# Kernel optimization log

Measured on AMD Instinct MI355X. Metric: run time of the kernel, lower is better.

The kernel has to match this reference:

```python
import jax, jax.numpy as jnp
import numpy as np

ALPHA = 0.2  # leakyrelu slope


def setup_inputs() -> dict:
    key = jax.random.key(0)
    ks = jax.random.split(key, 10)
    B, L, F, H, D = 16, 1024, 128, 4, 64
    HD = H * D  # 256
    s = lambda fan: 1.0 / np.sqrt(fan)
    return {
        "x":  jax.random.normal(ks[0], (B, L, F), jnp.float32),
        "W":  jax.random.normal(ks[1], (H, F, D), jnp.float32) * s(F),
        "a1": jax.random.normal(ks[2], (H, D), jnp.float32) * s(2 * D),
        "a2": jax.random.normal(ks[3], (H, D), jnp.float32) * s(2 * D),
        "Wq": jax.random.normal(ks[4], (HD, HD), jnp.float32) * s(HD),
        "bq": jnp.zeros((HD,), jnp.float32),
        "Wk": jax.random.normal(ks[5], (HD, HD), jnp.float32) * s(HD),
        "bk": jnp.zeros((HD,), jnp.float32),
        "Wv": jax.random.normal(ks[6], (HD, HD), jnp.float32) * s(HD),
        "bv": jnp.zeros((HD,), jnp.float32),
        "Wfc": jax.random.normal(ks[7], (HD, D), jnp.float32) * s(HD),
        "bfc": jnp.zeros((D,), jnp.float32),
    }


def reference(x, W, a1, a2, Wq, bq, Wk, bk, Wv, bv, Wfc, bfc):
    # ---- multi-head GAT (dense, all-pairs over seq_len) ----
    # Wh: [H, B, L, D]
    Wh = jnp.einsum('blf,hfd->hbld', x, W)
    # e_ij = leakyrelu(a1.Wh_i + a2.Wh_j)  (split of a over the concat)
    si = jnp.einsum('hbld,hd->hbl', Wh, a1)  # source term
    sj = jnp.einsum('hbld,hd->hbl', Wh, a2)  # target term
    e = jax.nn.leaky_relu(si[..., :, None] + sj[..., None, :], negative_slope=ALPHA)
    gat_att = jax.nn.softmax(e, axis=-1)               # [H,B,L,L]
    # dropout is identity in eval mode (training=False)
    h = jnp.einsum('hblm,hbmd->hbld', gat_att, Wh)     # [H,B,L,D]
    # concat heads -> [B, L, H*D]
    Hh, B, L, D = h.shape
    gat_out = jnp.transpose(h, (1, 2, 0, 3)).reshape(B, L, Hh * D)

    # ---- temporal attention over the concatenated features ----
    Q = gat_out @ Wq + bq
    K = gat_out @ Wk + bk
    V = gat_out @ Wv + bv
    scale = 1.0 / np.sqrt(Hh * D)
    scores = jnp.einsum('bld,bmd->blm', Q, K) * scale
    t_att = jax.nn.softmax(scores, axis=-1)            # [B,L,L]
    temporal_out = jnp.einsum('blm,bmd->bld', t_att, V)

    # ---- output projection (dropout identity in eval) ----
    out = temporal_out @ Wfc + bfc                     # [B,L,D]
    return (out, gat_att, t_att, temporal_out)
```

## Files before the change

### kernel.cpp

```cpp
#include <hip/hip_runtime.h>


constexpr int Bc = 16, Lc = 1024, Fc = 128, Hc = 4, Dc = 64, HDc = 256;
constexpr int Nrows = Bc * Lc;
#define ALPHA_SLOPE 0.2f

typedef __attribute__((ext_vector_type(8))) short bf16x8;
typedef __attribute__((ext_vector_type(4))) float f32x4;

enum { A_F32 = 0, A_HL = 1 };
enum { E_BIAS = 1, E_WHT = 2, E_STATS = 3, E_QKV = 4 };

__device__ __forceinline__ float lrelu(float x) { return x > 0.f ? x : ALPHA_SLOPE * x; }

__device__ __forceinline__ void gll16(const void* g, void* l) {
    __builtin_amdgcn_global_load_lds(
        (const __attribute__((address_space(1))) void*)g,
        (__attribute__((address_space(3))) void*)l, 16, 0, 0);
}

__device__ __forceinline__ void split2(float a, float b, unsigned& h, unsigned& l) {
    const unsigned ua = __float_as_uint(a), ub = __float_as_uint(b);
    h = __byte_perm(ua, ub, 0x7632);
    const float la = a - __uint_as_float(ua & 0xffff0000u);
    const float lb = b - __uint_as_float(ub & 0xffff0000u);
    l = __byte_perm(__float_as_uint(la), __float_as_uint(lb), 0x7632);
}
__device__ __forceinline__ void split1(float v, unsigned short& h, unsigned short& l) {
    const unsigned u = __float_as_uint(v);
    h = (unsigned short)(u >> 16);
    const float lf = v - __uint_as_float(u & 0xffff0000u);
    l = (unsigned short)(__float_as_uint(lf) >> 16);
}

template <int BM, int BN, int AMODE, int EPI>
__global__ __launch_bounds__(256, 2) void mm_k(
    const float* __restrict__ Af,
    const unsigned short* __restrict__ Agh, const unsigned short* __restrict__ Agl,
    const unsigned short* __restrict__ Bgh, const unsigned short* __restrict__ Bgl,
    const float* __restrict__ bias,
    float* __restrict__ Cf,
    unsigned short* __restrict__ Ch, unsigned short* __restrict__ Cl,
    unsigned short* __restrict__ Ch2, unsigned short* __restrict__ Cl2,
    unsigned short* __restrict__ Ch3, unsigned short* __restrict__ Cl3,
    int K, int lda, int ldb, int ldc,
    long long zA, long long zB, long long zC, float alpha,
    const float* __restrict__ a1, const float* __restrict__ a2,
    float* __restrict__ si, float* __restrict__ sj, float* __restrict__ pstats)
{
    constexpr int ABUF = BM * 32, BBUF = BN * 32;
    __shared__ __align__(16) unsigned short SM[4 * ABUF + 4 * BBUF];
    unsigned short* const Ah_s = SM;
    unsigned short* const Al_s = SM + 2 * ABUF;
    unsigned short* const Bh_s = SM + 4 * ABUF;
    unsigned short* const Bl_s = SM + 4 * ABUF + 2 * BBUF;

    constexpr bool SWAPXY = (EPI == E_QKV);

    const int nbx = gridDim.x, nby = gridDim.y;
    int lin = blockIdx.x + nbx * (blockIdx.y + nby * blockIdx.z);
    const int ntot = nbx * nby * gridDim.z;
    lin = (lin & 7) * (ntot >> 3) + (lin >> 3);
    const int bx = lin % nbx;
    const int rem = lin / nbx;
    const int by = rem % nby;
    const int z  = rem / nby;

    if (AMODE == A_F32) { Af += (size_t)z * zA; }
    else { Agh += (size_t)z * zA; Agl += (size_t)z * zA; }
    Bgh += (size_t)z * zB; Bgl += (size_t)z * zB;
    if (Cf) Cf += (size_t)z * zC;

    constexpr int WC = (BN == 64) ? 1 : 2, WR = 4 / WC;
    constexpr int WM = BM / WR, WN = BN / WC, MF = WM / 16, NF = WN / 16;
    const int row0 = (SWAPXY ? by : bx) * BM;
    const int col0 = (SWAPXY ? bx : by) * BN;
    const int t = threadIdx.x, lane = t & 63, wid = t >> 6;
    const int fr = lane & 15, g = lane >> 4, fk = g * 8;
    const int wrow = (wid / WC) * WM, wcol = (wid % WC) * WN;
    const int rsub = lane >> 2, cbyt = (lane & 3) * 16;

    f32x4 acc[MF][NF] = {};

    auto stageB = [&](int k0, int pp) {
        #pragma unroll
        for (int q = 0; q < BN / 64; ++q) {
            const int r = wid * (BN / 4) + q * 16;
            const size_t gb = ((size_t)(col0 + r + rsub) * ldb + k0) * 2 + cbyt;
            gll16((const char*)Bgh + gb, (char*)(Bh_s + pp * BBUF) + (size_t)r * 64);
            gll16((const char*)Bgl + gb, (char*)(Bl_s + pp * BBUF) + (size_t)r * 64);
        }
    };
    auto stageA = [&](int k0, int pp) {
        if (AMODE == A_HL) {
            #pragma unroll
            for (int q = 0; q < BM / 64; ++q) {
                const int r = wid * (BM / 4) + q * 16;
                const size_t gb = ((size_t)(row0 + r + rsub) * lda + k0) * 2 + cbyt;
                gll16((const char*)Agh + gb, (char*)(Ah_s + pp * ABUF) + (size_t)r * 64);
                gll16((const char*)Agl + gb, (char*)(Al_s + pp * ABUF) + (size_t)r * 64);
            }
        } else {
            const int r = t >> 1, h2 = t & 1;
            const float* srcA = Af + (size_t)(row0 + r) * lda + k0 + h2 * 16;
            const float4 v0 = ((const float4*)srcA)[0];
            const float4 v1 = ((const float4*)srcA)[1];
            const float4 v2 = ((const float4*)srcA)[2];
            const float4 v3 = ((const float4*)srcA)[3];
            unsigned hu[8], lu[8];
            split2(v0.x, v0.y, hu[0], lu[0]); split2(v0.z, v0.w, hu[1], lu[1]);
            split2(v1.x, v1.y, hu[2], lu[2]); split2(v1.z, v1.w, hu[3], lu[3]);
            split2(v2.x, v2.y, hu[4], lu[4]); split2(v2.z, v2.w, hu[5], lu[5]);
            split2(v3.x, v3.y, hu[6], lu[6]); split2(v3.z, v3.w, hu[7], lu[7]);
            uint4* dh = (uint4*)(Ah_s + pp * ABUF + r * 32 + h2 * 16);
            dh[0] = make_uint4(hu[0], hu[1], hu[2], hu[3]);
            dh[1] = make_uint4(hu[4], hu[5], hu[6], hu[7]);
            uint4* dl = (uint4*)(Al_s + pp * ABUF + r * 32 + h2 * 16);
            dl[0] = make_uint4(lu[0], lu[1], lu[2], lu[3]);
            dl[1] = make_uint4(lu[4], lu[5], lu[6], lu[7]);
        }
    };

    stageB(0, 0);
    stageA(0, 0);
    __syncthreads();

    const int NT = K / 32;
    int p = 0;
    for (int kt = 0; kt < NT; ++kt) {
        if (kt + 1 < NT) { stageB((kt + 1) * 32, p ^ 1); stageA((kt + 1) * 32, p ^ 1); }
        bf16x8 ah[MF], al[MF];
        #pragma unroll
        for (int mf = 0; mf < MF; ++mf) {
            const int off = p * ABUF + (wrow + mf * 16 + fr) * 32 + fk;
            ah[mf] = *(const bf16x8*)(Ah_s + off);
            al[mf] = *(const bf16x8*)(Al_s + off);
        }
        #pragma unroll
        for (int nf = 0; nf < NF; ++nf) {
            const int off = p * BBUF + (wcol + nf * 16 + fr) * 32 + fk;
            const bf16x8 bh = *(const bf16x8*)(Bh_s + off);
            const bf16x8 bl = *(const bf16x8*)(Bl_s + off);
            #pragma unroll
            for (int mf = 0; mf < MF; ++mf) {
                acc[mf][nf] = __builtin_amdgcn_mfma_f32_16x16x32_bf16(ah[mf], bh, acc[mf][nf], 0, 0, 0);
                acc[mf][nf] = __builtin_amdgcn_mfma_f32_16x16x32_bf16(al[mf], bh, acc[mf][nf], 0, 0, 0);
                acc[mf][nf] = __builtin_amdgcn_mfma_f32_16x16x32_bf16(ah[mf], bl, acc[mf][nf], 0, 0, 0);
            }
        }
        __syncthreads();
        p ^= 1;
    }

    float* ts = (float*)SM;

    if (EPI == E_BIAS || EPI == E_STATS) {
        float bv_[NF];
        if (EPI == E_BIAS) {
            #pragma unroll
            for (int nf = 0; nf < NF; ++nf) bv_[nf] = bias[col0 + wcol + nf * 16 + fr];
        }
        #pragma unroll
        for (int mf = 0; mf < MF; ++mf) {
            #pragma unroll
            for (int i = 0; i < 4; ++i) {
                const size_t row = (size_t)row0 + wrow + mf * 16 + g * 4 + i;
                const size_t co = row * ldc + col0 + wcol + fr;
                #pragma unroll
                for (int nf = 0; nf < NF; ++nf) {
                    float v = acc[mf][nf][i];
                    if (EPI == E_STATS) v *= alpha;
                    if (EPI == E_BIAS)  v += bv_[nf];
                    acc[mf][nf][i] = v;
                    Cf[co + nf * 16] = v;
                }
            }
        }
        if (EPI == E_STATS) {
            const int ty = by * WC + (wid % WC);
            #pragma unroll
            for (int mf = 0; mf < MF; ++mf) {
                #pragma unroll
                for (int i = 0; i < 4; ++i) {
                    float m = acc[mf][0][i], s;
                    #pragma unroll
                    for (int nf = 1; nf < NF; ++nf) m = fmaxf(m, acc[mf][nf][i]);
                    s = 0.f;
                    #pragma unroll
                    for (int nf = 0; nf < NF; ++nf) s += __expf(acc[mf][nf][i] - m);
                    #pragma unroll
                    for (int ofs = 1; ofs < 16; ofs <<= 1) {
                        const float om = __shfl_xor(m, ofs, 64);
                        const float os = __shfl_xor(s, ofs, 64);
                        const float nm = fmaxf(m, om);
                        s = s * __expf(m - nm) + os * __expf(om - nm);
                        m = nm;
                    }
                    if (fr == 0) {
                        const size_t row = (size_t)row0 + wrow + mf * 16 + g * 4 + i;
                        float* pp = pstats + (((size_t)z * 16 + ty) * Lc + row) * 2;
                        pp[0] = m; pp[1] = s;
                    }
                }
            }
        }
    }

    if (EPI == E_QKV) {
        float bv_[NF];
        #pragma unroll
        for (int nf = 0; nf < NF; ++nf) bv_[nf] = bias[col0 + wcol + nf * 16 + fr];
        #pragma unroll
        for (int mf = 0; mf < MF; ++mf)
            #pragma unroll
            for (int i = 0; i < 4; ++i)
                #pragma unroll
                for (int nf = 0; nf < NF; ++nf) acc[mf][nf][i] += bv_[nf];

        if (col0 < 512) {
            unsigned short* dH = (col0 < 256) ? Ch : Ch2;
            unsigned short* dL = (col0 < 256) ? Cl : Cl2;
            const int cl0 = col0 & 255;
            #pragma unroll
            for (int mf = 0; mf < MF; ++mf) {
                #pragma unroll
                for (int i = 0; i < 4; ++i) {
                    const size_t row = (size_t)row0 + wrow + mf * 16 + g * 4 + i;
                    const size_t co = row * ldc + cl0 + wcol + fr;
                    #pragma unroll
                    for (int nf = 0; nf < NF; ++nf) {
                        unsigned short hh16, ll16; split1(acc[mf][nf][i], hh16, ll16);
                        dH[co + nf * 16] = hh16; dL[co + nf * 16] = ll16;
                    }
                }
            }
        } else {
            const int bq_ = row0 >> 10, lg0 = row0 & 1023;
            #pragma unroll
            for (int hf = 0; hf < 2; ++hf) {
                if ((wid & 1) == hf) {
                    #pragma unroll
                    for (int mf = 0; mf < MF; ++mf)
                        #pragma unroll
                        for (int i = 0; i < 4; ++i) {
                            const int rr = wrow + mf * 16 + g * 4 + i;
                            #pragma unroll
                            for (int nf = 0; nf < NF; ++nf)
                                ts[rr * 65 + nf * 16 + fr] = acc[mf][nf][i];
                        }
                }
                __syncthreads();
                const int l = t & 127, db = (t >> 7) * 32;
                #pragma unroll
                for (int dd = 0; dd < 32; ++dd) {
                    const int dl = db + dd;
                    unsigned short hh16, ll16; split1(ts[l * 65 + dl], hh16, ll16);
                    const size_t o = ((size_t)bq_ * 256 + (col0 - 512) + hf * 64 + dl) * 1024 + lg0 + l;
                    Ch3[o] = hh16; Cl3[o] = ll16;
                }
                __syncthreads();
            }
        }
    }

    if (EPI == E_WHT) {
        float a1v[NF], a2v[NF];
        #pragma unroll
        for (int nf = 0; nf < NF; ++nf) {
            a1v[nf] = a1[(size_t)z * Dc + nf * 16 + fr];
            a2v[nf] = a2[(size_t)z * Dc + nf * 16 + fr];
        }
        #pragma unroll
        for (int mf = 0; mf < MF; ++mf) {
// ... 20 lines not shown
        #pragma unroll
        for (int mf = 0; mf < MF; ++mf)
            #pragma unroll
            for (int i = 0; i < 4; ++i) {
                const int rr = wrow + mf * 16 + g * 4 + i;
                #pragma unroll
                for (int nf = 0; nf < NF; ++nf)
                    ts[rr * 65 + nf * 16 + fr] = acc[mf][nf][i];
            }
        __syncthreads();
        const int bq_ = row0 >> 10, lg0 = row0 & 1023;
        const int l = t & 127, db = (t >> 7) * 32;
        #pragma unroll
        for (int dd = 0; dd < 32; ++dd) {
            const int d = db + dd;
            unsigned short hh16, ll16; split1(ts[l * 65 + d], hh16, ll16);
            const size_t o = (((size_t)(z * 16 + bq_)) * 64 + d) * 1024 + lg0 + l;
            Ch[o] = hh16; Cl[o] = ll16;
        }
    }
}

__global__ __launch_bounds__(256, 3) void gat_k(
    const float* __restrict__ si, const float* __restrict__ sj,
    const unsigned short* __restrict__ WhTh, const unsigned short* __restrict__ WhTl,
    float* __restrict__ att, unsigned short* __restrict__ gouth,
    unsigned short* __restrict__ goutl)
{
    constexpr int BBUF = 64 * 32;
    __shared__ __align__(16) unsigned short SMg[4 * BBUF];
    __shared__ __align__(16) float sjs[Lc];
    __shared__ float redm[4];
    unsigned short* const Bh_s = SMg;
    unsigned short* const Bl_s = SMg + 2 * BBUF;

    int lin = blockIdx.x + 8 * blockIdx.z;
    lin = (lin & 7) * 64 + (lin >> 3);
    const int bx = lin & 7, z = lin >> 3;

    const int row0 = bx * 128;
    const int t = threadIdx.x, lane = t & 63, wid = t >> 6;
    const int fr = lane & 15, g = lane >> 4, fk = g * 8;
    const int wrow = wid * 32;
    const int hh = z >> 4, bb = z & 15;
    const int rsub = lane >> 2, cbyt = (lane & 3) * 16;

    const unsigned short* WhTh_z = WhTh + (size_t)z * 64 * 1024;
    const unsigned short* WhTl_z = WhTl + (size_t)z * 64 * 1024;
    const float* sjz = sj + (size_t)z * 1024;
    float* attz = att + ((size_t)z * 1024 + row0) * 1024;

    auto stageB = [&](int j0, int pp) {
        const int r = wid * 16;
        const size_t gb = ((size_t)(r + rsub) * 1024 + j0) * 2 + cbyt;
        gll16((const char*)WhTh_z + gb, (char*)(Bh_s + pp * BBUF) + (size_t)r * 64);
        gll16((const char*)WhTl_z + gb, (char*)(Bl_s + pp * BBUF) + (size_t)r * 64);
    };

    stageB(0, 0);
    ((float4*)sjs)[t] = ((const float4*)sjz)[t];
    __syncthreads();

    {
        const float4 v = ((const float4*)sjs)[t];
        float m4 = fmaxf(fmaxf(v.x, v.y), fmaxf(v.z, v.w));
        #pragma unroll
        for (int ofs = 32; ofs >= 1; ofs >>= 1) m4 = fmaxf(m4, __shfl_xor(m4, ofs, 64));
        if (lane == 0) redm[wid] = m4;
    }
    __syncthreads();
    const float smax = fmaxf(fmaxf(redm[0], redm[1]), fmaxf(redm[2], redm[3]));
// ... 11 lines not shown
        for (int c = 0; c < 64; ++c) {
            const float4 w = sp[c];
            s += __expf(lrelu(sv + w.x) - mr[mf]) + __expf(lrelu(sv + w.y) - mr[mf])
               + __expf(lrelu(sv + w.z) - mr[mf]) + __expf(lrelu(sv + w.w) - mr[mf]);
        }
        s += __shfl_xor(s, 16, 64);
        s += __shfl_xor(s, 32, 64);
        inv[mf] = 1.0f / s;
    }

    f32x4 acc[2][4] = {};
    int p = 0;
    for (int kt = 0; kt < 32; ++kt) {
        const int j0 = kt * 32;
        if (kt < 31) stageB(j0 + 32, p ^ 1);
        bf16x8 ph[2], pl[2];
        #pragma unroll
        for (int mf = 0; mf < 2; ++mf) {
            const float4 s0 = ((const float4*)sjs)[(j0 >> 2) + g * 2];
            const float4 s1 = ((const float4*)sjs)[(j0 >> 2) + g * 2 + 1];
            float pr[8];
            pr[0] = __expf(lrelu(siv[mf] + s0.x) - mr[mf]) * inv[mf];
            pr[1] = __expf(lrelu(siv[mf] + s0.y) - mr[mf]) * inv[mf];
            pr[2] = __expf(lrelu(siv[mf] + s0.z) - mr[mf]) * inv[mf];
            pr[3] = __expf(lrelu(siv[mf] + s0.w) - mr[mf]) * inv[mf];
            pr[4] = __expf(lrelu(siv[mf] + s1.x) - mr[mf]) * inv[mf];
            pr[5] = __expf(lrelu(siv[mf] + s1.y) - mr[mf]) * inv[mf];
            pr[6] = __expf(lrelu(siv[mf] + s1.z) - mr[mf]) * inv[mf];
            pr[7] = __expf(lrelu(siv[mf] + s1.w) - mr[mf]) * inv[mf];
            float* ap = attz + (size_t)(wrow + mf * 16 + fr) * 1024 + j0 + fk;
            *(float4*)ap       = make_float4(pr[0], pr[1], pr[2], pr[3]);
            *(float4*)(ap + 4) = make_float4(pr[4], pr[5], pr[6], pr[7]);
            union { unsigned u[4]; bf16x8 v; } uh, ul;
            split2(pr[0], pr[1], uh.u[0], ul.u[0]);
            split2(pr[2], pr[3], uh.u[1], ul.u[1]);
            split2(pr[4], pr[5], uh.u[2], ul.u[2]);
            split2(pr[6], pr[7], uh.u[3], ul.u[3]);
            ph[mf] = uh.v; pl[mf] = ul.v;
        }
        #pragma unroll
        for (int nf = 0; nf < 4; ++nf) {
            const int off = p * BBUF + (nf * 16 + fr) * 32 + fk;
            const bf16x8 bh = *(const bf16x8*)(Bh_s + off);
            const bf16x8 bl = *(const bf16x8*)(Bl_s + off);
            #pragma unroll
            for (int mf = 0; mf < 2; ++mf) {
                acc[mf][nf] = __builtin_amdgcn_mfma_f32_16x16x32_bf16(ph[mf], bh, acc[mf][nf], 0, 0, 0);
                acc[mf][nf] = __builtin_amdgcn_mfma_f32_16x16x32_bf16(pl[mf], bh, acc[mf][nf], 0, 0, 0);
                acc[mf][nf] = __builtin_amdgcn_mfma_f32_16x16x32_bf16(ph[mf], bl, acc[mf][nf], 0, 0, 0);
            }
        }
        __syncthreads();
        p ^= 1;
    }
    #pragma unroll
    for (int mf = 0; mf < 2; ++mf) {
        #pragma unroll
        for (int i = 0; i < 4; ++i) {
            const int row_l = wrow + mf * 16 + g * 4 + i;
            const size_t base = ((size_t)bb * 1024 + row0 + row_l) * 256 + hh * 64 + fr;
            #pragma unroll
            for (int nf = 0; nf < 4; ++nf) {
                unsigned short hh16, ll16; split1(acc[mf][nf][i], hh16, ll16);
                gouth[base + nf * 16] = hh16;
                goutl[base + nf * 16] = ll16;
            }
        }
    }
}

__global__ __launch_bounds__(256, 2) void pv_k(
    float* __restrict__ scores, const float* __restrict__ pstats,
    const unsigned short* __restrict__ VTh, const unsigned short* __restrict__ VTl,
    const unsigned short* __restrict__ WfcTh, const unsigned short* __restrict__ WfcTl,
    const float* __restrict__ bfc,
    float* __restrict__ tout, float* __restrict__ outp)
{
    constexpr int ABUF = 32 * 32, BBUF = 256 * 32;
    __shared__ __align__(16) unsigned short SMp[4 * ABUF + 4 * BBUF];
    unsigned short* const Ah_s = SMp;
    unsigned short* const Al_s = SMp + 2 * ABUF;
    unsigned short* const Bh_s = SMp + 4 * ABUF;
    unsigned short* const Bl_s = SMp + 4 * ABUF + 2 * BBUF;

    int lin = blockIdx.x + 32 * blockIdx.z;
    lin = (lin & 7) * 64 + (lin >> 3);
    const int bx = lin & 31, z = lin >> 5;

    const int row0 = bx * 32;
    const int t = threadIdx.x, lane = t & 63, wid = t >> 6;
    const int fr = lane & 15, g = lane >> 4, fk = g * 8;
    const int rsub = lane >> 2, cbyt = (lane & 3) * 16;

    float* sc = scores + ((size_t)z * Lc + row0) * Lc;
    const unsigned short* VTh_z = VTh + (size_t)z * HDc * Lc;
    const unsigned short* VTl_z = VTl + (size_t)z * HDc * Lc;

    auto stageB = [&](int k0, int pp) {
        #pragma unroll
        for (int q = 0; q < 4; ++q) {
            const int r = q * 64 + wid * 16;
            const size_t gb = ((size_t)(r + rsub) * Lc + k0) * 2 + cbyt;
            gll16((const char*)VTh_z + gb, (char*)(Bh_s + pp * BBUF) + (size_t)r * 64);
            gll16((const char*)VTl_z + gb, (char*)(Bl_s + pp * BBUF) + (size_t)r * 64);
        }
    };

    stageB(0, 0);

    const int ar = t >> 3, cq = (t & 7) * 4;
    float m_ = -1e30f, s_ = 0.f;
    {
        const int q = t & 7;
        const float* pb = pstats + (((size_t)z * 16 + q * 2) * Lc + row0 + ar) * 2;
        #pragma unroll
        for (int j = 0; j < 2; ++j) {
            const float2 pp = *(const float2*)(pb + (size_t)j * Lc * 2);
            const float nm = fmaxf(m_, pp.x);
            s_ = s_ * __expf(m_ - nm) + pp.y * __expf(pp.x - nm);
// ... 6 lines not shown
            const float nm = fmaxf(m_, om);
            s_ = s_ * __expf(m_ - nm) + os * __expf(om - nm);
            m_ = nm;
        }
    }
    const float iv_ = 1.0f / s_;

    auto stageA = [&](int k0, int pp) {
        float* srcS = sc + (size_t)ar * Lc + k0 + cq;
        const float4 v0 = *(const float4*)srcS;
        float pr[4];
        pr[0] = __expf(v0.x - m_) * iv_; pr[1] = __expf(v0.y - m_) * iv_;
        pr[2] = __expf(v0.z - m_) * iv_; pr[3] = __expf(v0.w - m_) * iv_;
        *(float4*)srcS = make_float4(pr[0], pr[1], pr[2], pr[3]);
        unsigned hu[2], lu[2];
        split2(pr[0], pr[1], hu[0], lu[0]); split2(pr[2], pr[3], hu[1], lu[1]);
        *(uint2*)(Ah_s + pp * ABUF + ar * 32 + cq) = make_uint2(hu[0], hu[1]);
        *(uint2*)(Al_s + pp * ABUF + ar * 32 + cq) = make_uint2(lu[0], lu[1]);
    };

    f32x4 acc[2][4] = {};
    stageA(0, 0);
    __syncthreads();
    int p = 0;
    for (int kt = 0; kt < 32; ++kt) {
        if (kt < 31) { stageB((kt + 1) * 32, p ^ 1); stageA((kt + 1) * 32, p ^ 1); }
        bf16x8 ah[2], al[2];
        #pragma unroll
        for (int mf = 0; mf < 2; ++mf) {
            const int off = p * ABUF + (mf * 16 + fr) * 32 + fk;
            ah[mf] = *(const bf16x8*)(Ah_s + off);
            al[mf] = *(const bf16x8*)(Al_s + off);
        }
        #pragma unroll
        for (int nf = 0; nf < 4; ++nf) {
            const int off = p * BBUF + (wid * 64 + nf * 16 + fr) * 32 + fk;
            const bf16x8 bh = *(const bf16x8*)(Bh_s + off);
            const bf16x8 bl = *(const bf16x8*)(Bl_s + off);
            #pragma unroll
            for (int mf = 0; mf < 2; ++mf) {
                acc[mf][nf] = __builtin_amdgcn_mfma_f32_16x16x32_bf16(ah[mf], bh, acc[mf][nf], 0, 0, 0);
                acc[mf][nf] = __builtin_amdgcn_mfma_f32_16x16x32_bf16(al[mf], bh, acc[mf][nf], 0, 0, 0);
                acc[mf][nf] = __builtin_amdgcn_mfma_f32_16x16x32_bf16(ah[mf], bl, acc[mf][nf], 0, 0, 0);
            }
        }
        __syncthreads();
        p ^= 1;
    }

    constexpr int TS = 258;
    float* ts = (float*)SMp;
    #pragma unroll
    for (int mf = 0; mf < 2; ++mf) {
        #pragma unroll
        for (int i = 0; i < 4; ++i) {
            const size_t row = (size_t)row0 + mf * 16 + g * 4 + i;
            float* cp = tout + ((size_t)z * Lc + row) * HDc + wid * 64 + fr;
            #pragma unroll
            for (int nf = 0; nf < 4; ++nf) {
                cp[nf * 16] = acc[mf][nf][i];
                ts[(mf * 16 + g * 4 + i) * TS + wid * 64 + nf * 16 + fr] = acc[mf][nf][i];
            }
        }
    }
    __syncthreads();

    const int ocol = wid * 16 + fr;
    f32x4 acc2[2] = {};
    #pragma unroll
    for (int kt2 = 0; kt2 < 8; ++kt2) {
        const int kk = kt2 * 32 + fk;
        const bf16x8 bh = *(const bf16x8*)(WfcTh + ocol * 256 + kk);
        const bf16x8 bl = *(const bf16x8*)(WfcTl + ocol * 256 + kk);
        #pragma unroll
        for (int mf = 0; mf < 2; ++mf) {
            const float* ap = ts + (mf * 16 + fr) * TS + kk;
            union { unsigned u[4]; bf16x8 v; } ahh, all_;
            split2(ap[0], ap[1], ahh.u[0], all_.u[0]);
            split2(ap[2], ap[3], ahh.u[1], all_.u[1]);
            split2(ap[4], ap[5], ahh.u[2], all_.u[2]);
            split2(ap[6], ap[7], ahh.u[3], all_.u[3]);
            acc2[mf] = __builtin_amdgcn_mfma_f32_16x16x32_bf16(ahh.v, bh, acc2[mf], 0, 0, 0);
            acc2[mf] = __builtin_amdgcn_mfma_f32_16x16x32_bf16(all_.v, bh, acc2[mf], 0, 0, 0);
            acc2[mf] = __builtin_amdgcn_mfma_f32_16x16x32_bf16(ahh.v, bl, acc2[mf], 0, 0, 0);
        }
    }
    const float bo = bfc[ocol];
    #pragma unroll
    for (int mf = 0; mf < 2; ++mf)
        #pragma unroll
        for (int i = 0; i < 4; ++i)
            outp[((size_t)z * Lc + row0 + mf * 16 + g * 4 + i) * Dc + ocol] = acc2[mf][i] + bo;
}

__device__ __forceinline__ void tr32(const float* src, unsigned short* dh,
                                     unsigned short* dl, int R, int C,
                                     int r0, int c0, float (*tile)[33], int t)
{
    const int tc = t & 31, tr = t >> 5;
    #pragma unroll
    for (int rr = 0; rr < 32; rr += 8)
        tile[tr + rr][tc] = src[(size_t)(r0 + tr + rr) * C + c0 + tc];
    __syncthreads();
    #pragma unroll
    for (int rr = 0; rr < 32; rr += 8) {
        unsigned short h, l; split1(tile[tc][tr + rr], h, l);
        const size_t o = (size_t)(c0 + tr + rr) * R + r0 + tc;
        dh[o] = h; dl[o] = l;
    }
}

__global__ __launch_bounds__(256) void prep_k(
    const float* __restrict__ W, const float* __restrict__ Wq,
    const float* __restrict__ Wk, const float* __restrict__ Wv,
    const float* __restrict__ Wfc, const float* __restrict__ bq,
    const float* __restrict__ bk, const float* __restrict__ bv,
    unsigned short* __restrict__ WTh, unsigned short* __restrict__ WTl,
    unsigned short* __restrict__ Wch, unsigned short* __restrict__ Wcl,
    unsigned short* __restrict__ WfcTh, unsigned short* __restrict__ WfcTl,
    float* __restrict__ bcat)
{
    __shared__ float tile[32][33];
    const int bx = blockIdx.x, by = blockIdx.y, t = threadIdx.x;
    if (by == 0) {
        if (bx >= 32) return;
        const int h = bx >> 3, tl = bx & 7;
        tr32(W + (size_t)h * Fc * Dc, WTh + (size_t)h * Dc * Fc,
             WTl + (size_t)h * Dc * Fc, Fc, Dc, (tl >> 1) * 32, (tl & 1) * 32, tile, t);
    } else if (by <= 3) {
        const float* s = (by == 1) ? Wq : (by == 2) ? Wk : Wv;
        const size_t off = (size_t)(by - 1) * HDc * HDc;
        tr32(s, Wch + off, Wcl + off, HDc, HDc, (bx >> 3) * 32, (bx & 7) * 32, tile, t);
    } else {
        if (bx < 16) {
            tr32(Wfc, WfcTh, WfcTl, HDc, Dc, (bx >> 1) * 32, (bx & 1) * 32, tile, t);
        } else if (bx == 16) {
            bcat[t] = bq[t]; bcat[256 + t] = bk[t]; bcat[512 + t] = bv[t];
        }
    }
}

extern "C" void kernel_launch(void* const* d_in, const int* in_sizes, int n_in,
                              void* d_out, int out_size, void* d_ws, size_t ws_size,
                              hipStream_t stream)
{
    const float* x   = (const float*)d_in[0];
    const float* W   = (const float*)d_in[1];
    const float* a1  = (const float*)d_in[2];
    const float* a2  = (const float*)d_in[3];
    const float* Wq  = (const float*)d_in[4];
    const float* bq  = (const float*)d_in[5];
    const float* Wk  = (const float*)d_in[6];
    const float* bk  = (const float*)d_in[7];
    const float* Wv  = (const float*)d_in[8];
    const float* bv  = (const float*)d_in[9];
    const float* Wfc = (const float*)d_in[10];
    const float* bfc = (const float*)d_in[11];

    float* outp    = (float*)d_out;
    float* gat_att = outp + (size_t)Bc * Lc * Dc;
    float* t_att   = gat_att + (size_t)Hc * Bc * Lc * Lc;
    float* t_out   = t_att + (size_t)Bc * Lc * Lc;

    constexpr size_t MB = 1024 * 1024;
    char* wsb = (char*)d_ws;
    unsigned short* WhTh = (unsigned short*)wsb;
    unsigned short* WhTl = WhTh + (size_t)64 * 64 * 1024;
    unsigned short* VTh = WhTh; unsigned short* VTl = WhTl;
    unsigned short* gouth = (unsigned short*)(wsb + 16 * MB);
    unsigned short* goutl = gouth + (size_t)Nrows * HDc;
    unsigned short* Qh = (unsigned short*)(wsb + 32 * MB);
    unsigned short* Ql = Qh + (size_t)Nrows * HDc;
    unsigned short* Kh = (unsigned short*)(wsb + 48 * MB);
    unsigned short* Kl = Kh + (size_t)Nrows * HDc;
    float* si  = (float*)(wsb + 64 * MB);
    float* sj  = si + Hc * Nrows;
    float* pstats = sj + Hc * Nrows;
    unsigned short* WTh = (unsigned short*)(pstats + (size_t)Bc * 16 * Lc * 2);
    unsigned short* WTl = WTh + Hc * Dc * Fc;
    unsigned short* Wch = WTl + Hc * Dc * Fc;
    unsigned short* Wcl = Wch + 768 * HDc;
    unsigned short* WfcTh = Wcl + 768 * HDc;
    unsigned short* WfcTl = WfcTh + Dc * HDc;
    float* bcat = (float*)(WfcTl + Dc * HDc);

    const dim3 blk(256);

    prep_k<<<dim3(64, 5), blk, 0, stream>>>(W, Wq, Wk, Wv, Wfc, bq, bk, bv,
        WTh, WTl, Wch, Wcl, WfcTh, WfcTl, bcat);

    mm_k<128, 64, A_F32, E_WHT><<<dim3(Nrows / 128, 1, Hc), blk, 0, stream>>>(
        x, nullptr, nullptr, WTh, WTl, nullptr, nullptr,
        WhTh, WhTl, nullptr, nullptr, nullptr, nullptr,
        Fc, Fc, Fc, 0, 0LL, (long long)Dc * Fc, 0LL, 1.f, a1, a2, si, sj, nullptr);

    gat_k<<<dim3(Lc / 128, 1, 64), blk, 0, stream>>>(si, sj,
        WhTh, WhTl, gat_att, gouth, goutl);

    mm_k<128, 128, A_HL, E_QKV><<<dim3(6, Nrows / 128, 1), blk, 0, stream>>>(
        nullptr, gouth, goutl, Wch, Wcl, bcat, nullptr,
        Qh, Ql, Kh, Kl, VTh, VTl,
        HDc, HDc, HDc, HDc, 0LL, 0LL, 0LL, 1.f, nullptr, nullptr, nullptr, nullptr, nullptr);

    mm_k<128, 128, A_HL, E_STATS><<<dim3(8, 8, Bc), blk, 0, stream>>>(
        nullptr, Qh, Ql, Kh, Kl, nullptr, t_att,
        nullptr, nullptr, nullptr, nullptr, nullptr, nullptr,
        HDc, HDc, HDc, Lc, (long long)Lc * HDc, (long long)Lc * HDc,
        (long long)Lc * Lc, 0.0625f, nullptr, nullptr, nullptr, nullptr, pstats);

    pv_k<<<dim3(32, 1, Bc), blk, 0, stream>>>(t_att, pstats, VTh, VTl,
        WfcTh, WfcTl, bfc, t_out, outp);
}
```

Before: 235.2 us.

## Switch split-bf16 3-pass MFMA to fp16 hi/lo A with single fp16 B operand

Replaces the bf16 hi/lo emulation of fp32 GEMMs (three MFMAs per tile) with fp16: the A operand stays split into hi/lo fp16 while the B operand (weights, Wh, K, V) is stored as a single fp16. This removes one of three MFMAs per step, halves B-side LDS and global traffic, and shrinks the workspace for Wh, K and V. The cost is lower precision on the B side (fp16 mantissa, limited range), which could break tolerance if values overflow or need more bits.

```diff
diff --git a/kernel.cpp b/kernel.cpp
--- a/kernel.cpp
+++ b/kernel.cpp
@@ -5,11 +5,11 @@
 constexpr int Nrows = Bc * Lc;
 #define ALPHA_SLOPE 0.2f
 
-typedef __attribute__((ext_vector_type(8))) short bf16x8;
+typedef __attribute__((ext_vector_type(8))) _Float16 f16x8;
 typedef __attribute__((ext_vector_type(4))) float f32x4;
 
 enum { A_F32 = 0, A_HL = 1 };
-enum { E_BIAS = 1, E_WHT = 2, E_STATS = 3, E_QKV = 4 };
+enum { E_WHT = 2, E_STATS = 3, E_QKV = 4 };
 
 __device__ __forceinline__ float lrelu(float x) { return x > 0.f ? x : ALPHA_SLOPE * x; }
 
@@ -19,41 +19,43 @@
         (__attribute__((address_space(3))) void*)l, 16, 0, 0);
 }
 
-__device__ __forceinline__ void split2(float a, float b, unsigned& h, unsigned& l) {
-    const unsigned ua = __float_as_uint(a), ub = __float_as_uint(b);
-    h = __byte_perm(ua, ub, 0x7632);
-    const float la = a - __uint_as_float(ua & 0xffff0000u);
-    const float lb = b - __uint_as_float(ub & 0xffff0000u);
-    l = __byte_perm(__float_as_uint(la), __float_as_uint(lb), 0x7632);
-}
-__device__ __forceinline__ void split1(float v, unsigned short& h, unsigned short& l) {
-    const unsigned u = __float_as_uint(v);
-    h = (unsigned short)(u >> 16);
-    const float lf = v - __uint_as_float(u & 0xffff0000u);
-    l = (unsigned short)(__float_as_uint(lf) >> 16);
+__device__ __forceinline__ unsigned short cv1(float v) {
+    union { _Float16 f; unsigned short u; } c; c.f = (_Float16)v; return c.u;
+}
+__device__ __forceinline__ void sp2(float a, float b, unsigned& h, unsigned& l) {
+    const _Float16 ha = (_Float16)a, hb = (_Float16)b;
+    union { _Float16 f[2]; unsigned u; } H, L;
+    H.f[0] = ha; H.f[1] = hb;
+    L.f[0] = (_Float16)(a - (float)ha);
+    L.f[1] = (_Float16)(b - (float)hb);
+    h = H.u; l = L.u;
+}
+__device__ __forceinline__ void sp1(float v, unsigned short& h, unsigned short& l) {
+    const _Float16 hv = (_Float16)v;
+    union { _Float16 f; unsigned short u; } H, L;
+    H.f = hv; L.f = (_Float16)(v - (float)hv);
+    h = H.u; l = L.u;
 }
 
 template <int BM, int BN, int AMODE, int EPI>
 __global__ __launch_bounds__(256, 2) void mm_k(
     const float* __restrict__ Af,
     const unsigned short* __restrict__ Agh, const unsigned short* __restrict__ Agl,
-    const unsigned short* __restrict__ Bgh, const unsigned short* __restrict__ Bgl,
+    const unsigned short* __restrict__ Bg,
     const float* __restrict__ bias,
     float* __restrict__ Cf,
     unsigned short* __restrict__ Ch, unsigned short* __restrict__ Cl,
-    unsigned short* __restrict__ Ch2, unsigned short* __restrict__ Cl2,
-    unsigned short* __restrict__ Ch3, unsigned short* __restrict__ Cl3,
+    unsigned short* __restrict__ Ch2, unsigned short* __restrict__ Ch3,
     int K, int lda, int ldb, int ldc,
     long long zA, long long zB, long long zC, float alpha,
     const float* __restrict__ a1, const float* __restrict__ a2,
     float* __restrict__ si, float* __restrict__ sj, float* __restrict__ pstats)
 {
     constexpr int ABUF = BM * 32, BBUF = BN * 32;
-    __shared__ __align__(16) unsigned short SM[4 * ABUF + 4 * BBUF];
+    __shared__ __align__(16) unsigned short SM[4 * ABUF + 2 * BBUF];
     unsigned short* const Ah_s = SM;
     unsigned short* const Al_s = SM + 2 * ABUF;
-    unsigned short* const Bh_s = SM + 4 * ABUF;
-    unsigned short* const Bl_s = SM + 4 * ABUF + 2 * BBUF;
+    unsigned short* const Bf_s = SM + 4 * ABUF;
 
     constexpr bool SWAPXY = (EPI == E_QKV);
 
@@ -68,7 +70,7 @@
 
     if (AMODE == A_F32) { Af += (size_t)z * zA; }
     else { Agh += (size_t)z * zA; Agl += (size_t)z * zA; }
-    Bgh += (size_t)z * zB; Bgl += (size_t)z * zB;
+    Bg += (size_t)z * zB;
     if (Cf) Cf += (size_t)z * zC;
 
     constexpr int WC = (BN == 64) ? 1 : 2, WR = 4 / WC;
@@ -87,8 +89,7 @@
         for (int q = 0; q < BN / 64; ++q) {
             const int r = wid * (BN / 4) + q * 16;
             const size_t gb = ((size_t)(col0 + r + rsub) * ldb + k0) * 2 + cbyt;
-            gll16((const char*)Bgh + gb, (char*)(Bh_s + pp * BBUF) + (size_t)r * 64);
-            gll16((const char*)Bgl + gb, (char*)(Bl_s + pp * BBUF) + (size_t)r * 64);
+            gll16((const char*)Bg + gb, (char*)(Bf_s + pp * BBUF) + (size_t)r * 64);
         }
     };
     auto stageA = [&](int k0, int pp) {
@@ -108,10 +109,10 @@
             const float4 v2 = ((const float4*)srcA)[2];
             const float4 v3 = ((const float4*)srcA)[3];
             unsigned hu[8], lu[8];
-            split2(v0.x, v0.y, hu[0], lu[0]); split2(v0.z, v0.w, hu[1], lu[1]);
-            split2(v1.x, v1.y, hu[2], lu[2]); split2(v1.z, v1.w, hu[3], lu[3]);
-            split2(v2.x, v2.y, hu[4], lu[4]); split2(v2.z, v2.w, hu[5], lu[5]);
-            split2(v3.x, v3.y, hu[6], lu[6]); split2(v3.z, v3.w, hu[7], lu[7]);
+            sp2(v0.x, v0.y, hu[0], lu[0]); sp2(v0.z, v0.w, hu[1], lu[1]);
+            sp2(v1.x, v1.y, hu[2], lu[2]); sp2(v1.z, v1.w, hu[3], lu[3]);
+            sp2(v2.x, v2.y, hu[4], lu[4]); sp2(v2.z, v2.w, hu[5], lu[5]);
+            sp2(v3.x, v3.y, hu[6], lu[6]); sp2(v3.z, v3.w, hu[7], lu[7]);
             uint4* dh = (uint4*)(Ah_s + pp * ABUF + r * 32 + h2 * 16);
             dh[0] = make_uint4(hu[0], hu[1], hu[2], hu[3]);
             dh[1] = make_uint4(hu[4], hu[5], hu[6], hu[7]);
@@ -129,23 +130,21 @@
     int p = 0;
     for (int kt = 0; kt < NT; ++kt) {
         if (kt + 1 < NT) { stageB((kt + 1) * 32, p ^ 1); stageA((kt + 1) * 32, p ^ 1); }
-        bf16x8 ah[MF], al[MF];
+        f16x8 ah[MF], al[MF];
         #pragma unroll
         for (int mf = 0; mf < MF; ++mf) {
             const int off = p * ABUF + (wrow + mf * 16 + fr) * 32 + fk;
-            ah[mf] = *(const bf16x8*)(Ah_s + off);
-            al[mf] = *(const bf16x8*)(Al_s + off);
+            ah[mf] = *(const f16x8*)(Ah_s + off);
+            al[mf] = *(const f16x8*)(Al_s + off);
         }
         #pragma unroll
         for (int nf = 0; nf < NF; ++nf) {
             const int off = p * BBUF + (wcol + nf * 16 + fr) * 32 + fk;
-            const bf16x8 bh = *(const bf16x8*)(Bh_s + off);
-            const bf16x8 bl = *(const bf16x8*)(Bl_s + off);
+            const f16x8 bf = *(const f16x8*)(Bf_s + off);
             #pragma unroll
             for (int mf = 0; mf < MF; ++mf) {
-                acc[mf][nf] = __builtin_amdgcn_mfma_f32_16x16x32_bf16(ah[mf], bh, acc[mf][nf], 0, 0, 0);
-                acc[mf][nf] = __builtin_amdgcn_mfma_f32_16x16x32_bf16(al[mf], bh, acc[mf][nf], 0, 0, 0);
-                acc[mf][nf] = __builtin_amdgcn_mfma_f32_16x16x32_bf16(ah[mf], bl, acc[mf][nf], 0, 0, 0);
+                acc[mf][nf] = __builtin_amdgcn_mfma_f32_16x16x32_f16(ah[mf], bf, acc[mf][nf], 0, 0, 0);
+                acc[mf][nf] = __builtin_amdgcn_mfma_f32_16x16x32_f16(al[mf], bf, acc[mf][nf], 0, 0, 0);
             }
         }
         __syncthreads();
@@ -154,12 +153,7 @@
 
     float* ts = (float*)SM;
 
-    if (EPI == E_BIAS || EPI == E_STATS) {
-        float bv_[NF];
-        if (EPI == E_BIAS) {
-            #pragma unroll
-            for (int nf = 0; nf < NF; ++nf) bv_[nf] = bias[col0 + wcol + nf * 16 + fr];
-        }
+    if (EPI == E_STATS) {
         #pragma unroll
         for (int mf = 0; mf < MF; ++mf) {
             #pragma unroll
@@ -168,39 +162,35 @@
                 const size_t co = row * ldc + col0 + wcol + fr;
                 #pragma unroll
                 for (int nf = 0; nf < NF; ++nf) {
-                    float v = acc[mf][nf][i];
-                    if (EPI == E_STATS) v *= alpha;
-                    if (EPI == E_BIAS)  v += bv_[nf];
+                    float v = acc[mf][nf][i] * alpha;
                     acc[mf][nf][i] = v;
                     Cf[co + nf * 16] = v;
                 }
             }
         }
-        if (EPI == E_STATS) {
-            const int ty = by * WC + (wid % WC);
-            #pragma unroll
-            for (int mf = 0; mf < MF; ++mf) {
-                #pragma unroll
-                for (int i = 0; i < 4; ++i) {
-                    float m = acc[mf][0][i], s;
-                    #pragma unroll
-                    for (int nf = 1; nf < NF; ++nf) m = fmaxf(m, acc[mf][nf][i]);
-                    s = 0.f;
-                    #pragma unroll
-                    for (int nf = 0; nf < NF; ++nf) s += __expf(acc[mf][nf][i] - m);
-                    #pragma unroll
-                    for (int ofs = 1; ofs < 16; ofs <<= 1) {
-                        const float om = __shfl_xor(m, ofs, 64);
-                        const float os = __shfl_xor(s, ofs, 64);
-                        const float nm = fmaxf(m, om);
-                        s = s * __expf(m - nm) + os * __expf(om - nm);
-                        m = nm;
-                    }
-                    if (fr == 0) {
-                        const size_t row = (size_t)row0 + wrow + mf * 16 + g * 4 + i;
-                        float* pp = pstats + (((size_t)z * 16 + ty) * Lc + row) * 2;
-                        pp[0] = m; pp[1] = s;
-                    }
+        const int ty = by * WC + (wid % WC);
+        #pragma unroll
+        for (int mf = 0; mf < MF; ++mf) {
+            #pragma unroll
+            for (int i = 0; i < 4; ++i) {
+                float m = acc[mf][0][i], s;
+                #pragma unroll
+                for (int nf = 1; nf < NF; ++nf) m = fmaxf(m, acc[mf][nf][i]);
+                s = 0.f;
+                #pragma unroll
+                for (int nf = 0; nf < NF; ++nf) s += __expf(acc[mf][nf][i] - m);
+                #pragma unroll
+                for (int ofs = 1; ofs < 16; ofs <<= 1) {
+                    const float om = __shfl_xor(m, ofs, 64);
+                    const float os = __shfl_xor(s, ofs, 64);
+                    const float nm = fmaxf(m, om);
+                    s = s * __expf(m - nm) + os * __expf(om - nm);
+                    m = nm;
+                }
+                if (fr == 0) {
+                    const size_t row = (size_t)row0 + wrow + mf * 16 + g * 4 + i;
+                    float* pp = pstats + (((size_t)z * 16 + ty) * Lc + row) * 2;
+                    pp[0] = m; pp[1] = s;
                 }
             }
         }
@@ -217,9 +207,21 @@
                 #pragma unroll
                 for (int nf = 0; nf < NF; ++nf) acc[mf][nf][i] += bv_[nf];
 
-        if (col0 < 512) {
-            unsigned short* dH = (col0 < 256) ? Ch : Ch2;
-            unsigned short* dL = (col0 < 256) ? Cl : Cl2;
+        if (col0 < 256) {
+            #pragma unroll
+            for (int mf = 0; mf < MF; ++mf) {
+                #pragma unroll
+                for (int i = 0; i < 4; ++i) {
+                    const size_t row = (size_t)row0 + wrow + mf * 16 + g * 4 + i;
+                    const size_t co = row * ldc + col0 + wcol + fr;
+                    #pragma unroll
+                    for (int nf = 0; nf < NF; ++nf) {
+                        unsigned short hh16, ll16; sp1(acc[mf][nf][i], hh16, ll16);
+                        Ch[co + nf * 16] = hh16; Cl[co + nf * 16] = ll16;
+                    }
+                }
+            }
+        } else if (col0 < 512) {
             const int cl0 = col0 & 255;
             #pragma unroll
             for (int mf = 0; mf < MF; ++mf) {
@@ -228,10 +230,8 @@
                     const size_t row = (size_t)row0 + wrow + mf * 16 + g * 4 + i;
                     const size_t co = row * ldc + cl0 + wcol + fr;
                     #pragma unroll
-                    for (int nf = 0; nf < NF; ++nf) {
-                        unsigned short hh16, ll16; split1(acc[mf][nf][i], hh16, ll16);
-                        dH[co + nf * 16] = hh16; dL[co + nf * 16] = ll16;
-                    }
+                    for (int nf = 0; nf < NF; ++nf)
+                        Ch2[co + nf * 16] = cv1(acc[mf][nf][i]);
                 }
             }
         } else {
@@ -254,9 +254,8 @@
                 #pragma unroll
                 for (int dd = 0; dd < 32; ++dd) {
                     const int dl = db + dd;
-                    unsigned short hh16, ll16; split1(ts[l * 65 + dl], hh16, ll16);
                     const size_t o = ((size_t)bq_ * 256 + (col0 - 512) + hf * 64 + dl) * 1024 + lg0 + l;
-                    Ch3[o] = hh16; Cl3[o] = ll16;
+                    Ch3[o] = cv1(ts[l * 65 + dl]);
                 }
                 __syncthreads();
             }
@@ -307,25 +306,23 @@
         #pragma unroll
         for (int dd = 0; dd < 32; ++dd) {
             const int d = db + dd;
-            unsigned short hh16, ll16; split1(ts[l * 65 + d], hh16, ll16);
             const size_t o = (((size_t)(z * 16 + bq_)) * 64 + d) * 1024 + lg0 + l;
-            Ch[o] = hh16; Cl[o] = ll16;
+            Ch[o] = cv1(ts[l * 65 + d]);
         }
     }
 }
 
 __global__ __launch_bounds__(256, 3) void gat_k(
     const float* __restrict__ si, const float* __restrict__ sj,
-    const unsigned short* __restrict__ WhTh, const unsigned short* __restrict__ WhTl,
+    const unsigned short* __restrict__ WhTf,
     float* __restrict__ att, unsigned short* __restrict__ gouth,
     unsigned short* __restrict__ goutl)
 {
     constexpr int BBUF = 64 * 32;
-    __shared__ __align__(16) unsigned short SMg[4 * BBUF];
+    __shared__ __align__(16) unsigned short SMg[2 * BBUF];
     __shared__ __align__(16) float sjs[Lc];
     __shared__ float redm[4];
-    unsigned short* const Bh_s = SMg;
-    unsigned short* const Bl_s = SMg + 2 * BBUF;
+    unsigned short* const Bf_s = SMg;
 
     int lin = blockIdx.x + 8 * blockIdx.z;
     lin = (lin & 7) * 64 + (lin >> 3);
@@ -338,16 +335,14 @@
     const int hh = z >> 4, bb = z & 15;
     const int rsub = lane >> 2, cbyt = (lane & 3) * 16;
 
-    const unsigned short* WhTh_z = WhTh + (size_t)z * 64 * 1024;
-    const unsigned short* WhTl_z = WhTl + (size_t)z * 64 * 1024;
+    const unsigned short* WhTf_z = WhTf + (size_t)z * 64 * 1024;
     const float* sjz = sj + (size_t)z * 1024;
     float* attz = att + ((size_t)z * 1024 + row0) * 1024;
 
     auto stageB = [&](int j0, int pp) {
         const int r = wid * 16;
         const size_t gb = ((size_t)(r + rsub) * 1024 + j0) * 2 + cbyt;
-        gll16((const char*)WhTh_z + gb, (char*)(Bh_s + pp * BBUF) + (size_t)r * 64);
-        gll16((const char*)WhTl_z + gb, (char*)(Bl_s + pp * BBUF) + (size_t)r * 64);
+        gll16((const char*)WhTf_z + gb, (char*)(Bf_s + pp * BBUF) + (size_t)r * 64);
     };
 
     stageB(0, 0);
@@ -389,7 +384,7 @@
     for (int kt = 0; kt < 32; ++kt) {
         const int j0 = kt * 32;
         if (kt < 31) stageB(j0 + 32, p ^ 1);
-        bf16x8 ph[2], pl[2];
+        f16x8 ph[2], pl[2];
         #pragma unroll
         for (int mf = 0; mf < 2; ++mf) {
             const float4 s0 = ((const float4*)sjs)[(j0 >> 2) + g * 2];
@@ -406,23 +401,21 @@
             float* ap = attz + (size_t)(wrow + mf * 16 + fr) * 1024 + j0 + fk;
             *(float4*)ap       = make_float4(pr[0], pr[1], pr[2], pr[3]);
             *(float4*)(ap + 4) = make_float4(pr[4], pr[5], pr[6], pr[7]);
-            union { unsigned u[4]; bf16x8 v; } uh, ul;
-            split2(pr[0], pr[1], uh.u[0], ul.u[0]);
-            split2(pr[2], pr[3], uh.u[1], ul.u[1]);
-            split2(pr[4], pr[5], uh.u[2], ul.u[2]);
-            split2(pr[6], pr[7], uh.u[3], ul.u[3]);
+            union { unsigned u[4]; f16x8 v; } uh, ul;
+            sp2(pr[0], pr[1], uh.u[0], ul.u[0]);
+            sp2(pr[2], pr[3], uh.u[1], ul.u[1]);
+            sp2(pr[4], pr[5], uh.u[2], ul.u[2]);
+            sp2(pr[6], pr[7], uh.u[3], ul.u[3]);
             ph[mf] = uh.v; pl[mf] = ul.v;
         }
         #pragma unroll
         for (int nf = 0; nf < 4; ++nf) {
             const int off = p * BBUF + (nf * 16 + fr) * 32 + fk;
-            const bf16x8 bh = *(const bf16x8*)(Bh_s + off);
-            const bf16x8 bl = *(const bf16x8*)(Bl_s + off);
+            const f16x8 bf = *(const f16x8*)(Bf_s + off);
             #pragma unroll
             for (int mf = 0; mf < 2; ++mf) {
-                acc[mf][nf] = __builtin_amdgcn_mfma_f32_16x16x32_bf16(ph[mf], bh, acc[mf][nf], 0, 0, 0);
-                acc[mf][nf] = __builtin_amdgcn_mfma_f32_16x16x32_bf16(pl[mf], bh, acc[mf][nf], 0, 0, 0);
-                acc[mf][nf] = __builtin_amdgcn_mfma_f32_16x16x32_bf16(ph[mf], bl, acc[mf][nf], 0, 0, 0);
+                acc[mf][nf] = __builtin_amdgcn_mfma_f32_16x16x32_f16(ph[mf], bf, acc[mf][nf], 0, 0, 0);
+                acc[mf][nf] = __builtin_amdgcn_mfma_f32_16x16x32_f16(pl[mf], bf, acc[mf][nf], 0, 0, 0);
             }
         }
         __syncthreads();
@@ -436,7 +429,7 @@
             const size_t base = ((size_t)bb * 1024 + row0 + row_l) * 256 + hh * 64 + fr;
             #pragma unroll
             for (int nf = 0; nf < 4; ++nf) {
-                unsigned short hh16, ll16; split1(acc[mf][nf][i], hh16, ll16);
+                unsigned short hh16, ll16; sp1(acc[mf][nf][i], hh16, ll16);
                 gouth[base + nf * 16] = hh16;
                 goutl[base + nf * 16] = ll16;
             }
@@ -446,17 +439,15 @@
 
 __global__ __launch_bounds__(256, 2) void pv_k(
     float* __restrict__ scores, const float* __restrict__ pstats,
-    const unsigned short* __restrict__ VTh, const unsigned short* __restrict__ VTl,
-    const unsigned short* __restrict__ WfcTh, const unsigned short* __restrict__ WfcTl,
-    const float* __restrict__ bfc,
+    const unsigned short* __restrict__ VTf,
+    const unsigned short* __restrict__ WfcTf, const float* __restrict__ bfc,
     float* __restrict__ tout, float* __restrict__ outp)
 {
     constexpr int ABUF = 32 * 32, BBUF = 256 * 32;
-    __shared__ __align__(16) unsigned short SMp[4 * ABUF + 4 * BBUF];
+    __shared__ __align__(16) unsigned short SMp[4 * ABUF + 2 * BBUF];
     unsigned short* const Ah_s = SMp;
     unsigned short* const Al_s = SMp + 2 * ABUF;
-    unsigned short* const Bh_s = SMp + 4 * ABUF;
-    unsigned short* const Bl_s = SMp + 4 * ABUF + 2 * BBUF;
+    unsigned short* const Bf_s = SMp + 4 * ABUF;
 
     int lin = blockIdx.x + 32 * blockIdx.z;
     lin = (lin & 7) * 64 + (lin >> 3);
@@ -468,16 +459,14 @@
     const int rsub = lane >> 2, cbyt = (lane & 3) * 16;
 
     float* sc = scores + ((size_t)z * Lc + row0) * Lc;
-    const unsigned short* VTh_z = VTh + (size_t)z * HDc * Lc;
-    const unsigned short* VTl_z = VTl + (size_t)z * HDc * Lc;
+    const unsigned short* VTf_z = VTf + (size_t)z * HDc * Lc;
 
     auto stageB = [&](int k0, int pp) {
         #pragma unroll
         for (int q = 0; q < 4; ++q) {
             const int r = q * 64 + wid * 16;
             const size_t gb = ((size_t)(r + rsub) * Lc + k0) * 2 + cbyt;
-            gll16((const char*)VTh_z + gb, (char*)(Bh_s + pp * BBUF) + (size_t)r * 64);
-            gll16((const char*)VTl_z + gb, (char*)(Bl_s + pp * BBUF) + (size_t)r * 64);
+            gll16((const char*)VTf_z + gb, (char*)(Bf_s + pp * BBUF) + (size_t)r * 64);
         }
     };
 
@@ -514,7 +503,7 @@
         pr[2] = __expf(v0.z - m_) * iv_; pr[3] = __expf(v0.w - m_) * iv_;
         *(float4*)srcS = make_float4(pr[0], pr[1], pr[2], pr[3]);
         unsigned hu[2], lu[2];
-        split2(pr[0], pr[1], hu[0], lu[0]); split2(pr[2], pr[3], hu[1], lu[1]);
+        sp2(pr[0], pr[1], hu[0], lu[0]); sp2(pr[2], pr[3], hu[1], lu[1]);
         *(uint2*)(Ah_s + pp * ABUF + ar * 32 + cq) = make_uint2(hu[0], hu[1]);
         *(uint2*)(Al_s + pp * ABUF + ar * 32 + cq) = make_uint2(lu[0], lu[1]);
     };
@@ -525,23 +514,21 @@
     int p = 0;
     for (int kt = 0; kt < 32; ++kt) {
         if (kt < 31) { stageB((kt + 1) * 32, p ^ 1); stageA((kt + 1) * 32, p ^ 1); }
-        bf16x8 ah[2], al[2];
+        f16x8 ah[2], al[2];
         #pragma unroll
         for (int mf = 0; mf < 2; ++mf) {
             const int off = p * ABUF + (mf * 16 + fr) * 32 + fk;
-            ah[mf] = *(const bf16x8*)(Ah_s + off);
-            al[mf] = *(const bf16x8*)(Al_s + off);
+            ah[mf] = *(const f16x8*)(Ah_s + off);
+            al[mf] = *(const f16x8*)(Al_s + off);
         }
         #pragma unroll
         for (int nf = 0; nf < 4; ++nf) {
             const int off = p * BBUF + (wid * 64 + nf * 16 + fr) * 32 + fk;
-            const bf16x8 bh = *(const bf16x8*)(Bh_s + off);
-            const bf16x8 bl = *(const bf16x8*)(Bl_s + off);
+            const f16x8 bf = *(const f16x8*)(Bf_s + off);
             #pragma unroll
             for (int mf = 0; mf < 2; ++mf) {
-                acc[mf][nf] = __builtin_amdgcn_mfma_f32_16x16x32_bf16(ah[mf], bh, acc[mf][nf], 0, 0, 0);
-                acc[mf][nf] = __builtin_amdgcn_mfma_f32_16x16x32_bf16(al[mf], bh, acc[mf][nf], 0, 0, 0);
-                acc[mf][nf] = __builtin_amdgcn_mfma_f32_16x16x32_bf16(ah[mf], bl, acc[mf][nf], 0, 0, 0);
+                acc[mf][nf] = __builtin_amdgcn_mfma_f32_16x16x32_f16(ah[mf], bf, acc[mf][nf], 0, 0, 0);
+                acc[mf][nf] = __builtin_amdgcn_mfma_f32_16x16x32_f16(al[mf], bf, acc[mf][nf], 0, 0, 0);
             }
         }
         __syncthreads();
@@ -570,19 +557,17 @@
     #pragma unroll
     for (int kt2 = 0; kt2 < 8; ++kt2) {
         const int kk = kt2 * 32 + fk;
-        const bf16x8 bh = *(const bf16x8*)(WfcTh + ocol * 256 + kk);
-        const bf16x8 bl = *(const bf16x8*)(WfcTl + ocol * 256 + kk);
+        const f16x8 bf = *(const f16x8*)(WfcTf + ocol * 256 + kk);
         #pragma unroll
         for (int mf = 0; mf < 2; ++mf) {
             const float* ap = ts + (mf * 16 + fr) * TS + kk;
-            union { unsigned u[4]; bf16x8 v; } ahh, all_;
-            split2(ap[0], ap[1], ahh.u[0], all_.u[0]);
-            split2(ap[2], ap[3], ahh.u[1], all_.u[1]);
-            split2(ap[4], ap[5], ahh.u[2], all_.u[2]);
-            split2(ap[6], ap[7], ahh.u[3], all_.u[3]);
-            acc2[mf] = __builtin_amdgcn_mfma_f32_16x16x32_bf16(ahh.v, bh, acc2[mf], 0, 0, 0);
-            acc2[mf] = __builtin_amdgcn_mfma_f32_16x16x32_bf16(all_.v, bh, acc2[mf], 0, 0, 0);
-            acc2[mf] = __builtin_amdgcn_mfma_f32_16x16x32_bf16(ahh.v, bl, acc2[mf], 0, 0, 0);
+            union { unsigned u[4]; f16x8 v; } ahh, all_;
+            sp2(ap[0], ap[1], ahh.u[0], all_.u[0]);
+            sp2(ap[2], ap[3], ahh.u[1], all_.u[1]);
+            sp2(ap[4], ap[5], ahh.u[2], all_.u[2]);
+            sp2(ap[6], ap[7], ahh.u[3], all_.u[3]);
+            acc2[mf] = __builtin_amdgcn_mfma_f32_16x16x32_f16(ahh.v, bf, acc2[mf], 0, 0, 0);
+            acc2[mf] = __builtin_amdgcn_mfma_f32_16x16x32_f16(all_.v, bf, acc2[mf], 0, 0, 0);
         }
     }
     const float bo = bfc[ocol];
@@ -594,8 +579,8 @@
 }
 
 __device__ __forceinline__ void tr32(const float* src, unsigned short* dh,
-                                     unsigned short* dl, int R, int C,
-                                     int r0, int c0, float (*tile)[33], int t)
+                                     int R, int C, int r0, int c0,
+                                     float (*tile)[33], int t)
 {
     const int tc = t & 31, tr = t >> 5;
     #pragma unroll
@@ -604,9 +589,8 @@
     __syncthreads();
     #pragma unroll
     for (int rr = 0; rr < 32; rr += 8) {
-        unsigned short h, l; split1(tile[tc][tr + rr], h, l);
         const size_t o = (size_t)(c0 + tr + rr) * R + r0 + tc;
-        dh[o] = h; dl[o] = l;
+        dh[o] = cv1(tile[tc][tr + rr]);
     }
 }
 
@@ -615,25 +599,23 @@
     const float* __restrict__ Wk, const float* __restrict__ Wv,
     const float* __restrict__ Wfc, const float* __restrict__ bq,
     const float* __restrict__ bk, const float* __restrict__ bv,
-    unsigned short* __restrict__ WTh, unsigned short* __restrict__ WTl,
-    unsigned short* __restrict__ Wch, unsigned short* __restrict__ Wcl,
-    unsigned short* __restrict__ WfcTh, unsigned short* __restrict__ WfcTl,
-    float* __restrict__ bcat)
+    unsigned short* __restrict__ WTf, unsigned short* __restrict__ Wcf,
+    unsigned short* __restrict__ WfcTf, float* __restrict__ bcat)
 {
     __shared__ float tile[32][33];
     const int bx = blockIdx.x, by = blockIdx.y, t = threadIdx.x;
     if (by == 0) {
         if (bx >= 32) return;
         const int h = bx >> 3, tl = bx & 7;
-        tr32(W + (size_t)h * Fc * Dc, WTh + (size_t)h * Dc * Fc,
-             WTl + (size_t)h * Dc * Fc, Fc, Dc, (tl >> 1) * 32, (tl & 1) * 32, tile, t);
+        tr32(W + (size_t)h * Fc * Dc, WTf + (size_t)h * Dc * Fc,
+             Fc, Dc, (tl >> 1) * 32, (tl & 1) * 32, tile, t);
     } else if (by <= 3) {
         const float* s = (by == 1) ? Wq : (by == 2) ? Wk : Wv;
         const size_t off = (size_t)(by - 1) * HDc * HDc;
-        tr32(s, Wch + off, Wcl + off, HDc, HDc, (bx >> 3) * 32, (bx & 7) * 32, tile, t);
+        tr32(s, Wcf + off, HDc, HDc, (bx >> 3) * 32, (bx & 7) * 32, tile, t);
     } else {
         if (bx < 16) {
-            tr32(Wfc, WfcTh, WfcTl, HDc, Dc, (bx >> 1) * 32, (bx & 1) * 32, tile, t);
+            tr32(Wfc, WfcTf, HDc, Dc, (bx >> 1) * 32, (bx & 1) * 32, tile, t);
         } else if (bx == 16) {
             bcat[t] = bq[t]; bcat[256 + t] = bk[t]; bcat[512 + t] = bv[t];
         }
@@ -664,50 +646,45 @@
 
     constexpr size_t MB = 1024 * 1024;
     char* wsb = (char*)d_ws;
-    unsigned short* WhTh = (unsigned short*)wsb;
-    unsigned short* WhTl = WhTh + (size_t)64 * 64 * 1024;
-    unsigned short* VTh = WhTh; unsigned short* VTl = WhTl;
-    unsigned short* gouth = (unsigned short*)(wsb + 16 * MB);
+    unsigned short* WhTf = (unsigned short*)wsb;
+    unsigned short* VTf  = WhTf;
+    unsigned short* gouth = (unsigned short*)(wsb + 8 * MB);
     unsigned short* goutl = gouth + (size_t)Nrows * HDc;
-    unsigned short* Qh = (unsigned short*)(wsb + 32 * MB);
+    unsigned short* Qh = (unsigned short*)(wsb + 24 * MB);
     unsigned short* Ql = Qh + (size_t)Nrows * HDc;
-    unsigned short* Kh = (unsigned short*)(wsb + 48 * MB);
-    unsigned short* Kl = Kh + (size_t)Nrows * HDc;
-    float* si  = (float*)(wsb + 64 * MB);
+    unsigned short* Kf = (unsigned short*)(wsb + 40 * MB);
+    float* si  = (float*)(wsb + 48 * MB);
     float* sj  = si + Hc * Nrows;
     float* pstats = sj + Hc * Nrows;
-    unsigned short* WTh = (unsigned short*)(pstats + (size_t)Bc * 16 * Lc * 2);
-    unsigned short* WTl = WTh + Hc * Dc * Fc;
-    unsigned short* Wch = WTl + Hc * Dc * Fc;
-    unsigned short* Wcl = Wch + 768 * HDc;
-    unsigned short* WfcTh = Wcl + 768 * HDc;
-    unsigned short* WfcTl = WfcTh + Dc * HDc;
-    float* bcat = (float*)(WfcTl + Dc * HDc);
+    unsigned short* WTf = (unsigned short*)(pstats + (size_t)Bc * 16 * Lc * 2);
+    unsigned short* Wcf = WTf + Hc * Dc * Fc;
+    unsigned short* WfcTf = Wcf + 768 * HDc;
+    float* bcat = (float*)(WfcTf + Dc * HDc);
 
     const dim3 blk(256);
 
     prep_k<<<dim3(64, 5), blk, 0, stream>>>(W, Wq, Wk, Wv, Wfc, bq, bk, bv,
-        WTh, WTl, Wch, Wcl, WfcTh, WfcTl, bcat);
+        WTf, Wcf, WfcTf, bcat);
 
     mm_k<128, 64, A_F32, E_WHT><<<dim3(Nrows / 128, 1, Hc), blk, 0, stream>>>(
-        x, nullptr, nullptr, WTh, WTl, nullptr, nullptr,
-        WhTh, WhTl, nullptr, nullptr, nullptr, nullptr,
+        x, nullptr, nullptr, WTf, nullptr, nullptr,
+        WhTf, nullptr, nullptr, nullptr,
         Fc, Fc, Fc, 0, 0LL, (long long)Dc * Fc, 0LL, 1.f, a1, a2, si, sj, nullptr);
 
     gat_k<<<dim3(Lc / 128, 1, 64), blk, 0, stream>>>(si, sj,
-        WhTh, WhTl, gat_att, gouth, goutl);
+        WhTf, gat_att, gouth, goutl);
 
     mm_k<128, 128, A_HL, E_QKV><<<dim3(6, Nrows / 128, 1), blk, 0, stream>>>(
-        nullptr, gouth, goutl, Wch, Wcl, bcat, nullptr,
-        Qh, Ql, Kh, Kl, VTh, VTl,
+        nullptr, gouth, goutl, Wcf, bcat, nullptr,
+        Qh, Ql, Kf, VTf,
         HDc, HDc, HDc, HDc, 0LL, 0LL, 0LL, 1.f, nullptr, nullptr, nullptr, nullptr, nullptr);
 
     mm_k<128, 128, A_HL, E_STATS><<<dim3(8, 8, Bc), blk, 0, stream>>>(
-        nullptr, Qh, Ql, Kh, Kl, nullptr, t_att,
-        nullptr, nullptr, nullptr, nullptr, nullptr, nullptr,
+        nullptr, Qh, Ql, Kf, nullptr, t_att,
+        nullptr, nullptr, nullptr, nullptr,
         HDc, HDc, HDc, Lc, (long long)Lc * HDc, (long long)Lc * HDc,
         (long long)Lc * Lc, 0.0625f, nullptr, nullptr, nullptr, nullptr, pstats);
 
-    pv_k<<<dim3(32, 1, Bc), blk, 0, stream>>>(t_att, pstats, VTh, VTl,
-        WfcTh, WfcTl, bfc, t_out, outp);
-}
+    pv_k<<<dim3(32, 1, Bc), blk, 0, stream>>>(t_att, pstats, VTf,
+        WfcTf, bfc, t_out, outp);
+}
```

Result: faster. 194.6 us, median of 2 (-17.3%).
